# Optimization experiments

Measured on AMD Instinct MI355X. Metric: run time of the kernel, lower is better.

Reference implementation:

```python
import jax, jax.numpy as jnp
import numpy as np

B, S, D, M = 8, 32, 256, 2048
TOPK = 8

def setup_inputs() -> dict:
    key = jax.random.key(0)
    ks = jax.random.split(key, 10)
    def lin(kw, fan_in, fan_out):
        # kaiming normal (linear): std = 1/sqrt(fan_in); stored as [in, out]
        return jax.random.normal(kw, (fan_in, fan_out), jnp.float32) / jnp.sqrt(fan_in)
    return {
        "x": jax.random.normal(ks[0], (B, S, D), jnp.float32),
        "memory": jax.random.normal(ks[1], (M, D), jnp.float32) * 0.02,
        "Wq": lin(ks[2], D, D), "bq": jnp.zeros((D,), jnp.float32),
        "Wk": lin(ks[3], D, D), "bk": jnp.zeros((D,), jnp.float32),
        "Wv": lin(ks[4], D, D), "bv": jnp.zeros((D,), jnp.float32),
        "Wg": lin(ks[5], 2 * D, D), "bg": jnp.zeros((D,), jnp.float32),
    }

def reference(x, memory, Wq, bq, Wk, bk, Wv, bv, Wg, bg):
    batch, seq_len, d = x.shape
    scale = jnp.sqrt(jnp.float32(d))
    mem0 = jnp.broadcast_to(memory[None], (batch,) + memory.shape)  # [B,M,D]
    b_idx = jnp.arange(batch)[:, None]

    def step(mem, xt):  # mem [B,M,D], xt [B,D]
        q = xt @ Wq + bq                      # [B,D]
        k = mem @ Wk + bk                     # [B,M,D]
        v = mem @ Wv + bv                     # [B,M,D]
        logits = jnp.einsum('bd,bmd->bm', q, k) / scale
        attn = jax.nn.softmax(logits, axis=-1)            # [B,M]
        out = jnp.einsum('bm,bmd->bd', attn, v)           # [B,D]
        g = jax.nn.sigmoid(jnp.concatenate([xt, out], axis=-1) @ Wg + bg)  # [B,D]
        _, top_idx = jax.lax.top_k(attn, TOPK)            # [B,TOPK]
        old = jnp.take_along_axis(mem, top_idx[:, :, None], axis=1)        # [B,TOPK,D]
        new = (1.0 - g)[:, None, :] * old + g[:, None, :] * xt[:, None, :]
        mem = mem.at[b_idx, top_idx].set(new)
        return mem, out

    _, outs = jax.lax.scan(step, mem0, jnp.swapaxes(x, 0, 1))  # outs [S,B,D]
    return jnp.swapaxes(outs, 0, 1)  # [B,S,D]
```

## Files before the change

### kernel.cpp

```cpp
#include <hip/hip_runtime.h>
#include <math.h>

constexpr int B_ = 8, S_ = 32, D_ = 256, M_ = 2048;
constexpr int N_ = S_ * B_;
constexpr int TK = 8;
constexpr int NSLOT = 256;
constexpr int TOPC = 256;
constexpr int NCAND = NSLOT + TOPC;
constexpr int KSPLIT = 4;

__global__ __launch_bounds__(256) void k_wvwgT(const float* __restrict__ Wv,
                                               const float* __restrict__ Wg,
                                               const float* __restrict__ bv,
                                               const float* __restrict__ bg,
                                               const float* __restrict__ Wk,
                                               float* __restrict__ WvWgB,
                                               float* __restrict__ bvg,
                                               float* __restrict__ WkT) {
  int blk = blockIdx.x;
  int tid = threadIdx.x;
  if (blk >= 17) {
    __shared__ float tile[32][33];
    int bb = blk - 17;
    int bx = bb & 7, by = bb >> 3;
    int x0 = bx * 32, y0 = by * 32;
    int tx = tid & 31, ty = tid >> 5;
    for (int j = ty; j < 32; j += 8) tile[j][tx] = Wk[(y0 + j) * D_ + x0 + tx];
    __syncthreads();
    for (int j = ty; j < 32; j += 8) WkT[(x0 + j) * D_ + y0 + tx] = tile[tx][j];
    return;
  }
  if (blk == 16) {
    float a = bg[tid];
#pragma unroll 8
    for (int j = 0; j < D_; ++j) a = fmaf(bv[j], Wg[(size_t)(D_ + j) * D_ + tid], a);
    bvg[tid] = a;
    return;
  }
  int i0 = (blk & 3) * 64, d0 = (blk >> 2) * 64;
  __shared__ float At[64 * 64];
  __shared__ float Bt[64 * 64];
  const int r = tid & 63, c = tid >> 6;
  const int lane = tid & 63, wvv = tid >> 6;
  const int tx = lane & 15, ty = lane >> 4;
  const int dg = tx * 4, ig = (wvv * 4 + ty) * 4;
  float acc[4][4];
#pragma unroll
  for (int i = 0; i < 4; ++i)
#pragma unroll
    for (int j = 0; j < 4; ++j) acc[i][j] = 0.f;
  for (int kc = 0; kc < 4; ++kc) {
    __syncthreads();
#pragma unroll
    for (int it = 0; it < 4; ++it) {
      int jq = (c * 4 + it) * 4;
      float4 a = *(const float4*)&Wv[(i0 + r) * D_ + kc * 64 + jq];
      At[(jq + 0) * 64 + r] = a.x; At[(jq + 1) * 64 + r] = a.y;
      At[(jq + 2) * 64 + r] = a.z; At[(jq + 3) * 64 + r] = a.w;
      *(float4*)&Bt[r * 64 + jq] =
          *(const float4*)&Wg[(size_t)(D_ + kc * 64 + r) * D_ + d0 + jq];
    }
    __syncthreads();
#pragma unroll 4
    for (int j = 0; j < 64; ++j) {
      float4 av = *(const float4*)&At[j * 64 + ig];
      float4 bv4 = *(const float4*)&Bt[j * 64 + dg];
      acc[0][0] = fmaf(av.x, bv4.x, acc[0][0]); acc[0][1] = fmaf(av.x, bv4.y, acc[0][1]);
      acc[0][2] = fmaf(av.x, bv4.z, acc[0][2]); acc[0][3] = fmaf(av.x, bv4.w, acc[0][3]);
      acc[1][0] = fmaf(av.y, bv4.x, acc[1][0]); acc[1][1] = fmaf(av.y, bv4.y, acc[1][1]);
      acc[1][2] = fmaf(av.y, bv4.z, acc[1][2]); acc[1][3] = fmaf(av.y, bv4.w, acc[1][3]);
      acc[2][0] = fmaf(av.z, bv4.x, acc[2][0]); acc[2][1] = fmaf(av.z, bv4.y, acc[2][1]);
      acc[2][2] = fmaf(av.z, bv4.z, acc[2][2]); acc[2][3] = fmaf(av.z, bv4.w, acc[2][3]);
      acc[3][0] = fmaf(av.w, bv4.x, acc[3][0]); acc[3][1] = fmaf(av.w, bv4.y, acc[3][1]);
      acc[3][2] = fmaf(av.w, bv4.z, acc[3][2]); acc[3][3] = fmaf(av.w, bv4.w, acc[3][3]);
    }
  }
#pragma unroll
  for (int i = 0; i < 4; ++i)
    *(float4*)&WvWgB[(size_t)(i0 + ig + i) * D_ + d0 + dg] =
        make_float4(acc[i][0], acc[i][1], acc[i][2], acc[i][3]);
}

__global__ __launch_bounds__(256) void k_qproj(
    const float* __restrict__ x, const float* __restrict__ Wq,
    const float* __restrict__ bq, const float* __restrict__ bk,
    const float* __restrict__ WkT, const float* __restrict__ Wg,
    float* __restrict__ qt, float* __restrict__ qbk, float* __restrict__ xgp) {
  int n = blockIdx.x, tid = threadIdx.x;
  int t = n / B_, b = n % B_;
  __shared__ float xr[D_], qsh[D_];
  __shared__ float red[4];
  xr[tid] = x[(b * S_ + t) * D_ + tid];
  __syncthreads();
  float accq = bq[tid], accg = 0.f;
#pragma unroll 8
  for (int i = 0; i < D_; ++i) {
    float xv = xr[i];
    accq = fmaf(xv, Wq[i * D_ + tid], accq);
    accg = fmaf(xv, Wg[i * D_ + tid], accg);
  }
  qsh[tid] = accq;
  xgp[n * D_ + tid] = accg;
  float p = accq * bk[tid];
  for (int off = 32; off > 0; off >>= 1) p += __shfl_down(p, off, 64);
  if ((tid & 63) == 0) red[tid >> 6] = p;
  __syncthreads();
  float acct = 0.f;
#pragma unroll 8
  for (int i = 0; i < D_; ++i) acct = fmaf(qsh[i], WkT[i * D_ + tid], acct);
  qt[n * D_ + tid] = acct;
  if (tid == 0) qbk[n] = red[0] + red[1] + red[2] + red[3];
}

__global__ __launch_bounds__(256) void k_L0(
    const float* __restrict__ qt, const float* __restrict__ mem,
    const float* __restrict__ qbk, float* __restrict__ L0) {
  __shared__ float qtT[64 * 64];
  __shared__ float mT[64 * 64];
  const int tid = threadIdx.x;
  const int m0 = blockIdx.x * 64, n0 = blockIdx.y * 64;
  const int r = tid & 63, c = tid >> 6;
  const int lane = tid & 63, wv = tid >> 6;
  const int tx = lane & 15, ty = lane >> 4;
  const int mg = tx * 4, ng = (wv * 4 + ty) * 4;
  float acc[4][4];
#pragma unroll
  for (int i = 0; i < 4; ++i)
#pragma unroll
    for (int j = 0; j < 4; ++j) acc[i][j] = 0.f;
  for (int kc = 0; kc < 4; ++kc) {
    __syncthreads();
#pragma unroll
    for (int it = 0; it < 4; ++it) {
      int kq = (c * 4 + it) * 4;
      float4 a = *(const float4*)&qt[(n0 + r) * D_ + kc * 64 + kq];
      qtT[(kq + 0) * 64 + r] = a.x; qtT[(kq + 1) * 64 + r] = a.y;
      qtT[(kq + 2) * 64 + r] = a.z; qtT[(kq + 3) * 64 + r] = a.w;
      float4 bm = *(const float4*)&mem[(m0 + r) * D_ + kc * 64 + kq];
      mT[(kq + 0) * 64 + r] = bm.x; mT[(kq + 1) * 64 + r] = bm.y;
      mT[(kq + 2) * 64 + r] = bm.z; mT[(kq + 3) * 64 + r] = bm.w;
    }
    __syncthreads();
#pragma unroll 4
    for (int k = 0; k < 64; ++k) {
      float4 av = *(const float4*)&qtT[k * 64 + ng];
      float4 bv4 = *(const float4*)&mT[k * 64 + mg];
      acc[0][0] = fmaf(av.x, bv4.x, acc[0][0]); acc[0][1] = fmaf(av.x, bv4.y, acc[0][1]);
      acc[0][2] = fmaf(av.x, bv4.z, acc[0][2]); acc[0][3] = fmaf(av.x, bv4.w, acc[0][3]);
      acc[1][0] = fmaf(av.y, bv4.x, acc[1][0]); acc[1][1] = fmaf(av.y, bv4.y, acc[1][1]);
      acc[1][2] = fmaf(av.y, bv4.z, acc[1][2]); acc[1][3] = fmaf(av.y, bv4.w, acc[1][3]);
      acc[2][0] = fmaf(av.z, bv4.x, acc[2][0]); acc[2][1] = fmaf(av.z, bv4.y, acc[2][1]);
      acc[2][2] = fmaf(av.z, bv4.z, acc[2][2]); acc[2][3] = fmaf(av.z, bv4.w, acc[2][3]);
      acc[3][0] = fmaf(av.w, bv4.x, acc[3][0]); acc[3][1] = fmaf(av.w, bv4.y, acc[3][1]);
      acc[3][2] = fmaf(av.w, bv4.z, acc[3][2]); acc[3][3] = fmaf(av.w, bv4.w, acc[3][3]);
    }
  }
#pragma unroll
  for (int i = 0; i < 4; ++i) {
    int n = n0 + ng + i;
    float qbv = qbk[n];
    float4 o;
    o.x = (acc[i][0] + qbv) * 0.0625f; o.y = (acc[i][1] + qbv) * 0.0625f;
    o.z = (acc[i][2] + qbv) * 0.0625f; o.w = (acc[i][3] + qbv) * 0.0625f;
    *(float4*)&L0[n * M_ + m0 + mg] = o;
  }
}

__global__ __launch_bounds__(256) void k_sortstats(const float* __restrict__ L0,
                                                   float* __restrict__ topv,
                                                   int* __restrict__ topi,
                                                   float* __restrict__ M0,
                                                   double* __restrict__ SumE0) {
  int n = blockIdx.x, tid = threadIdx.x;
  __shared__ float v[M_];
  __shared__ short ix[M_];
  __shared__ double redd[4];
  for (int m = tid; m < M_; m += 256) {
    v[m] = L0[(size_t)n * M_ + m];
    ix[m] = (short)m;
  }
  __syncthreads();
  for (int size = 2; size <= M_; size <<= 1) {
    for (int stride = size >> 1; stride > 0; stride >>= 1) {
      for (int i = tid; i < M_ / 2; i += 256) {
        int pos = 2 * i - (i & (stride - 1));
        int j = pos + stride;
        bool desc = ((pos & size) == 0);
        float va = v[pos], vb2 = v[j];
        short ia = ix[pos], ib = ix[j];
        bool aG = (va > vb2) || (va == vb2 && ia < ib);
        if (desc ? !aG : aG) { v[pos] = vb2; v[j] = va; ix[pos] = ib; ix[j] = ia; }
      }
      __syncthreads();
    }
  }
  topv[n * TOPC + tid] = v[tid];
  topi[n * TOPC + tid] = (int)ix[tid];
  float mx = v[0];
  if (tid == 0) M0[n] = mx;
  double s = 0.0;
  for (int m = tid; m < M_; m += 256) s += (double)expf(v[m] - mx);
  for (int off = 32; off > 0; off >>= 1) s += __shfl_down(s, off, 64);
  if ((tid & 63) == 0) redd[tid >> 6] = s;
  __syncthreads();
  if (tid == 0) SumE0[n] = redd[0] + redd[1] + redd[2] + redd[3];
}

__global__ __launch_bounds__(256) void k_ctxpart(
    const float* __restrict__ L0, const float* __restrict__ M0,
    const float* __restrict__ mem, float* __restrict__ ctxp) {
  int ks = blockIdx.x;
  int n0 = blockIdx.y * 32;
  int d0 = blockIdx.z * 64;
  int tid = threadIdx.x;
  __shared__ float Et[64 * 32];
  __shared__ float mTl[64 * 64];
  __shared__ float Msh[32];
  if (tid < 32) Msh[tid] = M0[n0 + tid];
  const int lane = tid & 63, wv = tid >> 6;
  const int tx = lane & 15, ty = lane >> 4;
  const int ng = (wv * 4 + ty) * 2;
  const int dg = tx * 4;
  float acc[2][4] = {{0, 0, 0, 0}, {0, 0, 0, 0}};
  for (int kc = 0; kc < 8; ++kc) {
    int kb = ks * 512 + kc * 64;
    __syncthreads();
#pragma unroll
    for (int j = 0; j < 8; ++j) {
      int ii = tid + 256 * j;
      int nr = ii & 31, kk = ii >> 5;
      Et[kk * 32 + nr] = expf(L0[(n0 + nr) * M_ + kb + kk] - Msh[nr]);
    }
    {
      int r = tid & 63, c = tid >> 6;
#pragma unroll
      for (int j = 0; j < 4; ++j) {
        int c4 = (c * 4 + j) * 4;
        *(float4*)&mTl[r * 64 + c4] = *(const float4*)&mem[(kb + r) * D_ + d0 + c4];
      }
    }
    __syncthreads();
#pragma unroll 4
    for (int kk = 0; kk < 64; ++kk) {
      float4 mv = *(const float4*)&mTl[kk * 64 + dg];
      float e0v = Et[kk * 32 + ng], e1v = Et[kk * 32 + ng + 1];
      acc[0][0] = fmaf(e0v, mv.x, acc[0][0]); acc[0][1] = fmaf(e0v, mv.y, acc[0][1]);
      acc[0][2] = fmaf(e0v, mv.z, acc[0][2]); acc[0][3] = fmaf(e0v, mv.w, acc[0][3]);
      acc[1][0] = fmaf(e1v, mv.x, acc[1][0]); acc[1][1] = fmaf(e1v, mv.y, acc[1][1]);
      acc[1][2] = fmaf(e1v, mv.z, acc[1][2]); acc[1][3] = fmaf(e1v, mv.w, acc[1][3]);
    }
  }
#pragma unroll
  for (int i = 0; i < 2; ++i) {
    int n = n0 + ng + i;
    *(float4*)&ctxp[((size_t)ks * N_ + n) * D_ + d0 + dg] =
        make_float4(acc[i][0], acc[i][1], acc[i][2], acc[i][3]);
  }
}

__global__ __launch_bounds__(1024, 1) void k_scan(
    const float* __restrict__ x, const float* __restrict__ mem0,
    const float* __restrict__ Wv, const float* __restrict__ bv,
    const float* __restrict__ WvWgB, const float* __restrict__ bvg,
    const float* __restrict__ qt, const float* __restrict__ qbk,
    const float* __restrict__ xgp, const float* __restrict__ L0,
    const float* __restrict__ M0, const double* __restrict__ SumE0,
    const float* __restrict__ ctxp, const float* __restrict__ topv,
    const int* __restrict__ topi, float* __restrict__ memcur,
    float* __restrict__ out) {
  const int b = blockIdx.x;
  const int tid = threadIdx.x;
  const int lane = tid & 63;
  const int wvid = tid >> 6;

  __shared__ short tpos[M_];
  __shared__ int Tlist[NSLOT];
  __shared__ float candV[NCAND];
  __shared__ int candI[NCAND];
  __shared__ float dpart[15][D_];
  __shared__ float fpart[16][D_];
  __shared__ float fpart2[16][D_];
  __shared__ float utmp[TK][D_];
  __shared__ float qt_s[2][D_], xt_s[2][D_];
  __shared__ float CTX0_s[D_], xgp_s[D_], g_s[D_], bv_s[D_], bvg_s[D_];
  __shared__ float wvlds[64 * D_];
  __shared__ float Msc[S_], qbks[S_];
  __shared__ double sum0s[S_];
  __shared__ float redw[15];
  __shared__ float inv_esum;
  __shared__ int Tcount;
  __shared__ int selIdx[TK], selSlot[TK], selFresh[TK];

  const float4* mem04 = (const float4*)mem0;
  const float4* mcur4c = (const float4*)memcur;
  float4* mcur4 = (float4*)memcur;
  const float4* Wv4 = (const float4*)Wv;
  const float4* Wg4 = (const float4*)WvWgB;
  const float4* qt4 = (const float4*)qt;
  const float4* x4 = (const float4*)x;
  const float4* ctxp4 = (const float4*)ctxp;
  const float4* xgp4 = (const float4*)xgp;

  float4 wreg[16];
#pragma unroll
  for (int j = 0; j < 16; ++j) wreg[j] = Wv4[(size_t)(wvid * 16 + j) * 64 + lane];

  for (int m = tid; m < M_; m += 1024) tpos[m] = -1;
  for (int i = tid; i < 64 * 64; i += 1024)
    ((float4*)wvlds)[i] = Wg4[192 * 64 + i];
  if (tid < NCAND) {
    candV[tid] = -INFINITY;
    candI[tid] = 0x7FFFFFFF;
  }
  if (tid < S_) {
    Msc[tid] = M0[tid * B_ + b];
    qbks[tid] = qbk[tid * B_ + b];
    sum0s[tid] = SumE0[tid * B_ + b];
  } else if (tid >= 64 && tid < 64 + D_) {
    int d = tid - 64;
    bv_s[d] = bv[d];
    bvg_s[d] = bvg[d];
  } else if (tid >= 512 && tid < 576) {
    int j = tid - 512;
    ((float4*)qt_s[0])[j] = qt4[(size_t)b * 64 + j];
  } else if (tid >= 576 && tid < 640) {
    int j = tid - 576;
    ((float4*)xt_s[0])[j] = x4[(size_t)(b * S_) * 64 + j];
  }
  if (tid == 0) Tcount = 0;
  __syncthreads();

  for (int t = 0; t < S_; ++t) {
    const int n = t * B_ + b;
    const int par = t & 1;
    const int Tc = Tcount;
    const float c0 = Msc[t];
    const float qb = qbks[t];

    if (wvid < 15) {
      const float4 qv = ((const float4*)qt_s[par])[lane];
      float4 acc = make_float4(0.f, 0.f, 0.f, 0.f);
      float dsum = 0.f;
      int s = wvid;
      int m_c = 0;
      float4 mc_c = make_float4(0.f, 0.f, 0.f, 0.f), mo_c = mc_c;
      float l0_c = 0.f;
      if (s < Tc) {
        m_c = Tlist[s];
        mc_c = mcur4c[((size_t)(b * NSLOT + s)) * 64 + lane];
        mo_c = mem04[(size_t)m_c * 64 + lane];
        l0_c = L0[(size_t)n * M_ + m_c];
      }
      while (s < Tc) {
        const int s2 = s + 15;
        int m_n = 0;
        float4 mc_n = make_float4(0.f, 0.f, 0.f, 0.f), mo_n = mc_n;
        float l0_n = 0.f;
        if (s2 < Tc) {
          m_n = Tlist[s2];
          mc_n = mcur4c[((size_t)(b * NSLOT + s2)) * 64 + lane];
          mo_n = mem04[(size_t)m_n * 64 + lane];
          l0_n = L0[(size_t)n * M_ + m_n];
        }
        float p = mc_c.x * qv.x;
        p = fmaf(mc_c.y, qv.y, p);
        p = fmaf(mc_c.z, qv.z, p);
        p = fmaf(mc_c.w, qv.w, p);
#pragma unroll
        for (int off = 1; off < 64; off <<= 1) p += __shfl_xor(p, off, 64);
        const float cur = (p + qb) * 0.0625f;
        const float ce = expf(cur - c0);
        const float e0 = expf(l0_c - c0);
        acc.x = fmaf(ce, mc_c.x, acc.x); acc.x = fmaf(-e0, mo_c.x, acc.x);
        acc.y = fmaf(ce, mc_c.y, acc.y); acc.y = fmaf(-e0, mo_c.y, acc.y);
        acc.z = fmaf(ce, mc_c.z, acc.z); acc.z = fmaf(-e0, mo_c.z, acc.z);
        acc.w = fmaf(ce, mc_c.w, acc.w); acc.w = fmaf(-e0, mo_c.w, acc.w);
        dsum += ce - e0;
        if (lane == 0) {
          candV[s] = cur;
          candI[s] = m_c;
        }
        m_c = m_n; mc_c = mc_n; mo_c = mo_n; l0_c = l0_n;
        s = s2;
      }
      ((float4*)dpart[wvid])[lane] = acc;
      if (lane == 0) redw[wvid] = dsum;
    } else {
#pragma unroll
      for (int jj = 0; jj < 4; ++jj) {
        const int j = lane + jj * 64;
        const int ii = topi[n * TOPC + j];
        const bool fresh = (tpos[ii] < 0);
        candV[NSLOT + j] = fresh ? topv[n * TOPC + j] : -INFINITY;
        candI[NSLOT + j] = fresh ? ii : 0x7FFFFFFF;
      }
      const float4 c0v = ctxp4[(size_t)(0 * N_ + n) * 64 + lane];
      const float4 c1v = ctxp4[(size_t)(1 * N_ + n) * 64 + lane];
      const float4 c2v = ctxp4[(size_t)(2 * N_ + n) * 64 + lane];
      const float4 c3v = ctxp4[(size_t)(3 * N_ + n) * 64 + lane];
      ((float4*)CTX0_s)[lane] = make_float4(c0v.x + c1v.x + c2v.x + c3v.x,
                                            c0v.y + c1v.y + c2v.y + c3v.y,
                                            c0v.z + c1v.z + c2v.z + c3v.z,
                                            c0v.w + c1v.w + c2v.w + c3v.w);
      ((float4*)xgp_s)[lane] = xgp4[(size_t)n * 64 + lane];
      if (t + 1 < S_) {
        ((float4*)qt_s[par ^ 1])[lane] = qt4[(size_t)(n + B_) * 64 + lane];
        ((float4*)xt_s[par ^ 1])[lane] = x4[(size_t)(b * S_ + t + 1) * 64 + lane];
      }
    }
    __syncthreads();

    {
      float mynum = 0.f;
      if (lane < 16) {
        const int k = wvid * 16 + lane;
        float nv = CTX0_s[k];
#pragma unroll
        for (int p = 0; p < 15; ++p) nv += dpart[p][k];
        mynum = nv;
      }
      if (wvid == 15) {
        if (t + 1 < S_) {
          float cv[8];
          int ci[8];
#pragma unroll
          for (int j = 0; j < 8; ++j) {
            cv[j] = candV[lane * 8 + j];
            ci[j] = candI[lane * 8 + j];
          }
          for (int r = 0; r < TK; ++r) {
            float bvv = cv[0];
            int bii = ci[0];
#pragma unroll
            for (int j = 1; j < 8; ++j)
              if (cv[j] > bvv || (cv[j] == bvv && ci[j] < bii)) { bvv = cv[j]; bii = ci[j]; }
#pragma unroll
            for (int off = 1; off < 64; off <<= 1) {
              float ov = __shfl_xor(bvv, off, 64);
              int oi = __shfl_xor(bii, off, 64);
              if (ov > bvv || (ov == bvv && oi < bii)) { bvv = ov; bii = oi; }
            }
            if (lane == 0) selIdx[r] = bii;
#pragma unroll
            for (int j = 0; j < 8; ++j)
              if (ci[j] == bii) { cv[j] = -INFINITY; ci[j] = 0x7FFFFFFF; }
          }
          if (lane == 0) {
            int tc = Tcount;
            for (int k = 0; k < TK; ++k) {
              int m = selIdx[k];
              int s = tpos[m];
              if (s < 0) {
                s = tc++;
                tpos[m] = (short)s;
                Tlist[s] = m;
                selFresh[k] = 1;
              } else
                selFresh[k] = 0;
              selSlot[k] = s;
            }
            Tcount = tc;
          }
        }
        double ds = sum0s[t];
#pragma unroll
        for (int p = 0; p < 15; ++p) ds += (double)redw[p];
        if (lane == 0) inv_esum = (float)(1.0 / ds);
      }
      float4 a1 = make_float4(0.f, 0.f, 0.f, 0.f);
      float4 a2 = make_float4(0.f, 0.f, 0.f, 0.f);
      if (wvid >= 12) {
        const float4* wl = (const float4*)wvlds + (size_t)(wvid - 12) * 16 * 64;
#pragma unroll
        for (int j = 0; j < 16; ++j) {
          const float nv = __shfl(mynum, j, 64);
          a1.x = fmaf(nv, wreg[j].x, a1.x); a1.y = fmaf(nv, wreg[j].y, a1.y);
          a1.z = fmaf(nv, wreg[j].z, a1.z); a1.w = fmaf(nv, wreg[j].w, a1.w);
          const float4 w4 = wl[j * 64 + lane];
          a2.x = fmaf(nv, w4.x, a2.x); a2.y = fmaf(nv, w4.y, a2.y);
          a2.z = fmaf(nv, w4.z, a2.z); a2.w = fmaf(nv, w4.w, a2.w);
        }
      } else {
#pragma unroll
        for (int j = 0; j < 16; ++j) {
          const float nv = __shfl(mynum, j, 64);
          a1.x = fmaf(nv, wreg[j].x, a1.x); a1.y = fmaf(nv, wreg[j].y, a1.y);
          a1.z = fmaf(nv, wreg[j].z, a1.z); a1.w = fmaf(nv, wreg[j].w, a1.w);
          const float4 w4 = Wg4[(size_t)(wvid * 16 + j) * 64 + lane];
          a2.x = fmaf(nv, w4.x, a2.x); a2.y = fmaf(nv, w4.y, a2.y);
          a2.z = fmaf(nv, w4.z, a2.z); a2.w = fmaf(nv, w4.w, a2.w);
        }
      }
      ((float4*)fpart[wvid])[lane] = a1;
      ((float4*)fpart2[wvid])[lane] = a2;
    }
    __syncthreads();

    if (tid < D_) {
      float o = 0.f;
#pragma unroll
      for (int p = 0; p < 16; ++p) o += fpart[p][tid];
      o = o * inv_esum + bv_s[tid];
      out[((size_t)b * S_ + t) * D_ + tid] = o;
    } else if (tid < 2 * D_) {
      const int d = tid - D_;
      float gg = 0.f;
#pragma unroll
      for (int p = 0; p < 16; ++p) gg += fpart2[p][d];
      const float gin = xgp_s[d] + gg * inv_esum + bvg_s[d];
      g_s[d] = 1.0f / (1.0f + expf(-gin));
    } else if (tid >= 512 && t + 1 < S_) {
      const int j = tid - 512, k = j >> 6, l = j & 63;
      const int m = selIdx[k], s = selSlot[k];
      const float4 old4 = selFresh[k] ? mem04[(size_t)m * 64 + l]
                                      : mcur4c[((size_t)(b * NSLOT + s)) * 64 + l];
      ((float4*)utmp[k])[l] = old4;
    }
    __syncthreads();

    if (t + 1 < S_) {
      if (tid < 512) {
        const int k = tid >> 6, l = tid & 63;
        const int s = selSlot[k];
        const float4 old4 = ((const float4*)utmp[k])[l];
        const float4 g4 = ((const float4*)g_s)[l];
        const float4 xv = ((const float4*)xt_s[par])[l];
        float4 nw;
        nw.x = (1.0f - g4.x) * old4.x + g4.x * xv.x;
        nw.y = (1.0f - g4.y) * old4.y + g4.y * xv.y;
        nw.z = (1.0f - g4.z) * old4.z + g4.z * xv.z;
        nw.w = (1.0f - g4.w) * old4.w + g4.w * xv.w;
        mcur4[((size_t)(b * NSLOT + s)) * 64 + l] = nw;
      }
      __syncthreads();
    }
  }
}

extern "C" void kernel_launch(void* const* d_in, const int* in_sizes, int n_in,
                              void* d_out, int out_size, void* d_ws, size_t ws_size,
                              hipStream_t stream) {
  const float* x = (const float*)d_in[0];
  const float* mem0 = (const float*)d_in[1];
  const float* Wq = (const float*)d_in[2];
  const float* bq = (const float*)d_in[3];
  const float* Wk = (const float*)d_in[4];
  const float* bk = (const float*)d_in[5];
  const float* Wv = (const float*)d_in[6];
  const float* bv = (const float*)d_in[7];
  const float* Wg = (const float*)d_in[8];
  const float* bg = (const float*)d_in[9];
  float* out = (float*)d_out;
  float* ws = (float*)d_ws;

  size_t o = 0;
  float* WkT = ws + o;   o += (size_t)D_ * D_;
  float* qt = ws + o;    o += (size_t)N_ * D_;
  float* qbk = ws + o;   o += N_;
  float* xgp = ws + o;   o += (size_t)N_ * D_;
  float* L0 = ws + o;    o += (size_t)N_ * M_;
  float* M0 = ws + o;    o += N_;
  double* SumE0 = (double*)(ws + o); o += 2 * N_;
  float* ctxp = ws + o;  o += (size_t)KSPLIT * N_ * D_;
  float* topv = ws + o;  o += (size_t)N_ * TOPC;
  int* topi = (int*)(ws + o); o += (size_t)N_ * TOPC;
  float* WvWgB = ws + o; o += (size_t)D_ * D_;
  float* bvg = ws + o;   o += D_;
  float* memcur = ws + o; o += (size_t)B_ * NSLOT * D_;

  k_wvwgT<<<dim3(81), dim3(256), 0, stream>>>(Wv, Wg, bv, bg, Wk, WvWgB, bvg, WkT);
  k_qproj<<<dim3(N_), dim3(256), 0, stream>>>(x, Wq, bq, bk, WkT, Wg, qt, qbk, xgp);
  k_L0<<<dim3(M_ / 64, N_ / 64), dim3(256), 0, stream>>>(qt, mem0, qbk, L0);
  k_sortstats<<<dim3(N_), dim3(256), 0, stream>>>(L0, topv, topi, M0, SumE0);
  k_ctxpart<<<dim3(KSPLIT, N_ / 32, D_ / 64), dim3(256), 0, stream>>>(L0, M0, mem0, ctxp);
  k_scan<<<dim3(B_), dim3(1024), 0, stream>>>(x, mem0, Wv, bv, WvWgB, bvg, qt, qbk, xgp,
                                              L0, M0, SumE0, ctxp, topv, topi, memcur, out);
}
```

Baseline: 655.1 us.

## Defer memory slot updates into next step and restructure scan dot-product phase

The top-k memory row update is now deferred and fused into the next step's logit pass: each wave applies the pending gate blend as it loads the row, which removes two block-wide barriers and the utmp staging. The full 64-lane dot-product reduction becomes a 4-lane partial reduce written to LDS and summed per slot by separate threads. The corrections against the original memory rows move to 12 otherwise idle waves, and top-k selection runs in parallel with the accumulation. A new pre-kernel precomputes exp(L0 - max) so the scan does no exp per touched slot; in exchange it writes an extra N*M buffer and adds a barrier phase per step.

Result: slower. 799.1 us (+22.0%).

```diff
diff --git a/kernel.cpp b/kernel.cpp
--- a/kernel.cpp
+++ b/kernel.cpp
@@ -204,6 +204,19 @@
   if ((tid & 63) == 0) redd[tid >> 6] = s;
   __syncthreads();
   if (tid == 0) SumE0[n] = redd[0] + redd[1] + redd[2] + redd[3];
+}
+
+__global__ __launch_bounds__(256) void k_e0(const float* __restrict__ L0,
+                                            const float* __restrict__ M0,
+                                            float* __restrict__ E0all) {
+  int n = blockIdx.x;
+  float c = M0[n];
+  const float4* src = (const float4*)(L0 + (size_t)n * M_);
+  float4* dst = (float4*)(E0all + (size_t)n * M_);
+  for (int j = threadIdx.x; j < M_ / 4; j += 256) {
+    float4 v = src[j];
+    dst[j] = make_float4(expf(v.x - c), expf(v.y - c), expf(v.z - c), expf(v.w - c));
+  }
 }
 
 __global__ __launch_bounds__(256) void k_ctxpart(
@@ -263,7 +276,7 @@
     const float* __restrict__ Wv, const float* __restrict__ bv,
     const float* __restrict__ WvWgB, const float* __restrict__ bvg,
     const float* __restrict__ qt, const float* __restrict__ qbk,
-    const float* __restrict__ xgp, const float* __restrict__ L0,
+    const float* __restrict__ xgp, const float* __restrict__ E0all,
     const float* __restrict__ M0, const double* __restrict__ SumE0,
     const float* __restrict__ ctxp, const float* __restrict__ topv,
     const int* __restrict__ topi, float* __restrict__ memcur,
@@ -275,21 +288,22 @@
 
   __shared__ short tpos[M_];
   __shared__ int Tlist[NSLOT];
+  __shared__ int pendK[NSLOT];
   __shared__ float candV[NCAND];
   __shared__ int candI[NCAND];
-  __shared__ float dpart[15][D_];
+  __shared__ float pLDS[NSLOT * 17];
+  __shared__ float curE[NSLOT], e0sA[NSLOT], diffA[NSLOT];
+  __shared__ float dpart[16][D_];
   __shared__ float fpart[16][D_];
   __shared__ float fpart2[16][D_];
-  __shared__ float utmp[TK][D_];
   __shared__ float qt_s[2][D_], xt_s[2][D_];
   __shared__ float CTX0_s[D_], xgp_s[D_], g_s[D_], bv_s[D_], bvg_s[D_];
   __shared__ float wvlds[64 * D_];
   __shared__ float Msc[S_], qbks[S_];
   __shared__ double sum0s[S_];
-  __shared__ float redw[15];
   __shared__ float inv_esum;
   __shared__ int Tcount;
-  __shared__ int selIdx[TK], selSlot[TK], selFresh[TK];
+  __shared__ int selIdx[TK], selFresh[TK];
 
   const float4* mem04 = (const float4*)mem0;
   const float4* mcur4c = (const float4*)memcur;
@@ -306,6 +320,7 @@
   for (int j = 0; j < 16; ++j) wreg[j] = Wv4[(size_t)(wvid * 16 + j) * 64 + lane];
 
   for (int m = tid; m < M_; m += 1024) tpos[m] = -1;
+  for (int s = tid; s < NSLOT; s += 1024) pendK[s] = -1;
   for (int i = tid; i < 64 * 64; i += 1024)
     ((float4*)wvlds)[i] = Wg4[192 * 64 + i];
   if (tid < NCAND) {
@@ -336,55 +351,57 @@
     const int Tc = Tcount;
     const float c0 = Msc[t];
     const float qb = qbks[t];
+    const float* E0row = E0all + (size_t)n * M_;
 
     if (wvid < 15) {
       const float4 qv = ((const float4*)qt_s[par])[lane];
-      float4 acc = make_float4(0.f, 0.f, 0.f, 0.f);
-      float dsum = 0.f;
+      const float4 g4 = ((const float4*)g_s)[lane];
+      const float4 xpv = ((const float4*)xt_s[par ^ 1])[lane];
       int s = wvid;
-      int m_c = 0;
-      float4 mc_c = make_float4(0.f, 0.f, 0.f, 0.f), mo_c = mc_c;
-      float l0_c = 0.f;
       if (s < Tc) {
-        m_c = Tlist[s];
-        mc_c = mcur4c[((size_t)(b * NSLOT + s)) * 64 + lane];
-        mo_c = mem04[(size_t)m_c * 64 + lane];
-        l0_c = L0[(size_t)n * M_ + m_c];
-      }
-      while (s < Tc) {
-        const int s2 = s + 15;
-        int m_n = 0;
-        float4 mc_n = make_float4(0.f, 0.f, 0.f, 0.f), mo_n = mc_n;
-        float l0_n = 0.f;
-        if (s2 < Tc) {
-          m_n = Tlist[s2];
-          mc_n = mcur4c[((size_t)(b * NSLOT + s2)) * 64 + lane];
-          mo_n = mem04[(size_t)m_n * 64 + lane];
-          l0_n = L0[(size_t)n * M_ + m_n];
+        int m_c = Tlist[s];
+        int pk_c = pendK[s];
+        const float4* base_c = (pk_c >= 0 && selFresh[pk_c])
+                                   ? (mem04 + (size_t)m_c * 64)
+                                   : (mcur4c + ((size_t)(b * NSLOT + s)) * 64);
+        float4 row_c = base_c[lane];
+        while (true) {
+          const int s2 = s + 15;
+          int m_n = 0, pk_n = -1;
+          float4 row_n = make_float4(0.f, 0.f, 0.f, 0.f);
+          if (s2 < Tc) {
+            m_n = Tlist[s2];
+            pk_n = pendK[s2];
+            const float4* base_n = (pk_n >= 0 && selFresh[pk_n])
+                                       ? (mem04 + (size_t)m_n * 64)
+                                       : (mcur4c + ((size_t)(b * NSLOT + s2)) * 64);
+            row_n = base_n[lane];
+          }
+          float4 mc = row_c;
+          if (pk_c >= 0) {
+            mc.x = (1.0f - g4.x) * row_c.x + g4.x * xpv.x;
+            mc.y = (1.0f - g4.y) * row_c.y + g4.y * xpv.y;
+            mc.z = (1.0f - g4.z) * row_c.z + g4.z * xpv.z;
+            mc.w = (1.0f - g4.w) * row_c.w + g4.w * xpv.w;
+            mcur4[((size_t)(b * NSLOT + s)) * 64 + lane] = mc;
+            if (lane == 0) pendK[s] = -1;
+          }
+          float p = mc.x * qv.x;
+          p = fmaf(mc.y, qv.y, p);
+          p = fmaf(mc.z, qv.z, p);
+          p = fmaf(mc.w, qv.w, p);
+          p += __shfl_xor(p, 1, 64);
+          p += __shfl_xor(p, 2, 64);
+          if ((lane & 3) == 0) pLDS[s * 17 + (lane >> 2)] = p;
+          if (lane == 1) e0sA[s] = E0row[m_c];
+          if (lane == 2) candI[s] = m_c;
+          if (s2 >= Tc) break;
+          s = s2;
+          m_c = m_n;
+          pk_c = pk_n;
+          row_c = row_n;
         }
-        float p = mc_c.x * qv.x;
-        p = fmaf(mc_c.y, qv.y, p);
-        p = fmaf(mc_c.z, qv.z, p);
-        p = fmaf(mc_c.w, qv.w, p);
-#pragma unroll
-        for (int off = 1; off < 64; off <<= 1) p += __shfl_xor(p, off, 64);
-        const float cur = (p + qb) * 0.0625f;
-        const float ce = expf(cur - c0);
-        const float e0 = expf(l0_c - c0);
-        acc.x = fmaf(ce, mc_c.x, acc.x); acc.x = fmaf(-e0, mo_c.x, acc.x);
-        acc.y = fmaf(ce, mc_c.y, acc.y); acc.y = fmaf(-e0, mo_c.y, acc.y);
-        acc.z = fmaf(ce, mc_c.z, acc.z); acc.z = fmaf(-e0, mo_c.z, acc.z);
-        acc.w = fmaf(ce, mc_c.w, acc.w); acc.w = fmaf(-e0, mo_c.w, acc.w);
-        dsum += ce - e0;
-        if (lane == 0) {
-          candV[s] = cur;
-          candI[s] = m_c;
-        }
-        m_c = m_n; mc_c = mc_n; mo_c = mo_n; l0_c = l0_n;
-        s = s2;
-      }
-      ((float4*)dpart[wvid])[lane] = acc;
-      if (lane == 0) redw[wvid] = dsum;
+      }
     } else {
 #pragma unroll
       for (int jj = 0; jj < 4; ++jj) {
@@ -410,62 +427,103 @@
     }
     __syncthreads();
 
+    float4 accw = make_float4(0.f, 0.f, 0.f, 0.f);
+    if (tid < NSLOT) {
+      const int s = tid;
+      if (s < Tc) {
+        float dsum = 0.f;
+#pragma unroll
+        for (int j = 0; j < 16; ++j) dsum += pLDS[s * 17 + j];
+        const float cur = (dsum + qb) * 0.0625f;
+        const float ce = expf(cur - c0);
+        const float e0 = e0sA[s];
+        curE[s] = ce;
+        diffA[s] = ce - e0;
+        candV[s] = cur;
+      }
+    } else {
+      for (int s = wvid - 4; s < Tc; s += 12) {
+        const int m = Tlist[s];
+        const float e0 = e0sA[s];
+        const float4 mo = mem04[(size_t)m * 64 + lane];
+        accw.x = fmaf(-e0, mo.x, accw.x);
+        accw.y = fmaf(-e0, mo.y, accw.y);
+        accw.z = fmaf(-e0, mo.z, accw.z);
+        accw.w = fmaf(-e0, mo.w, accw.w);
+      }
+    }
+    __syncthreads();
+
+    if (wvid < 15) {
+      float4 acc = accw;
+      for (int s = wvid; s < Tc; s += 15) {
+        const float ce = curE[s];
+        const float4 mc = mcur4c[((size_t)(b * NSLOT + s)) * 64 + lane];
+        acc.x = fmaf(ce, mc.x, acc.x);
+        acc.y = fmaf(ce, mc.y, acc.y);
+        acc.z = fmaf(ce, mc.z, acc.z);
+        acc.w = fmaf(ce, mc.w, acc.w);
+      }
+      ((float4*)dpart[wvid])[lane] = acc;
+    } else {
+      ((float4*)dpart[15])[lane] = accw;
+      double ds = 0.0;
+      for (int s = lane; s < Tc; s += 64) ds += (double)diffA[s];
+      for (int off = 32; off > 0; off >>= 1) ds += __shfl_down(ds, off, 64);
+      if (lane == 0) inv_esum = (float)(1.0 / (sum0s[t] + ds));
+      if (t + 1 < S_) {
+        float cv[8];
+        int ci[8];
+#pragma unroll
+        for (int j = 0; j < 8; ++j) {
+          cv[j] = candV[lane * 8 + j];
+          ci[j] = candI[lane * 8 + j];
+        }
+        for (int r = 0; r < TK; ++r) {
+          float bvv = cv[0];
+          int bii = ci[0];
+#pragma unroll
+          for (int j = 1; j < 8; ++j)
+            if (cv[j] > bvv || (cv[j] == bvv && ci[j] < bii)) { bvv = cv[j]; bii = ci[j]; }
+#pragma unroll
+          for (int off = 1; off < 64; off <<= 1) {
+            float ov = __shfl_xor(bvv, off, 64);
+            int oi = __shfl_xor(bii, off, 64);
+            if (ov > bvv || (ov == bvv && oi < bii)) { bvv = ov; bii = oi; }
+          }
+          if (lane == 0) selIdx[r] = bii;
+#pragma unroll
+          for (int j = 0; j < 8; ++j)
+            if (ci[j] == bii) { cv[j] = -INFINITY; ci[j] = 0x7FFFFFFF; }
+        }
+        if (lane == 0) {
+          int tc = Tcount;
+          for (int k = 0; k < TK; ++k) {
+            const int m = selIdx[k];
+            int s = tpos[m];
+            if (s < 0) {
+              s = tc++;
+              tpos[m] = (short)s;
+              Tlist[s] = m;
+              selFresh[k] = 1;
+            } else
+              selFresh[k] = 0;
+            pendK[s] = k;
+          }
+          Tcount = tc;
+        }
+      }
+    }
+    __syncthreads();
+
     {
       float mynum = 0.f;
       if (lane < 16) {
         const int k = wvid * 16 + lane;
         float nv = CTX0_s[k];
 #pragma unroll
-        for (int p = 0; p < 15; ++p) nv += dpart[p][k];
+        for (int p = 0; p < 16; ++p) nv += dpart[p][k];
         mynum = nv;
-      }
-      if (wvid == 15) {
-        if (t + 1 < S_) {
-          float cv[8];
-          int ci[8];
-#pragma unroll
-          for (int j = 0; j < 8; ++j) {
-            cv[j] = candV[lane * 8 + j];
-            ci[j] = candI[lane * 8 + j];
-          }
-          for (int r = 0; r < TK; ++r) {
-            float bvv = cv[0];
-            int bii = ci[0];
-#pragma unroll
-            for (int j = 1; j < 8; ++j)
-              if (cv[j] > bvv || (cv[j] == bvv && ci[j] < bii)) { bvv = cv[j]; bii = ci[j]; }
-#pragma unroll
-            for (int off = 1; off < 64; off <<= 1) {
-              float ov = __shfl_xor(bvv, off, 64);
-              int oi = __shfl_xor(bii, off, 64);
-              if (ov > bvv || (ov == bvv && oi < bii)) { bvv = ov; bii = oi; }
-            }
-            if (lane == 0) selIdx[r] = bii;
-#pragma unroll
-            for (int j = 0; j < 8; ++j)
-              if (ci[j] == bii) { cv[j] = -INFINITY; ci[j] = 0x7FFFFFFF; }
-          }
-          if (lane == 0) {
-            int tc = Tcount;
-            for (int k = 0; k < TK; ++k) {
-              int m = selIdx[k];
-              int s = tpos[m];
-              if (s < 0) {
-                s = tc++;
-                tpos[m] = (short)s;
-                Tlist[s] = m;
-                selFresh[k] = 1;
-              } else
-                selFresh[k] = 0;
-              selSlot[k] = s;
-            }
-            Tcount = tc;
-          }
-        }
-        double ds = sum0s[t];
-#pragma unroll
-        for (int p = 0; p < 15; ++p) ds += (double)redw[p];
-        if (lane == 0) inv_esum = (float)(1.0 / ds);
       }
       float4 a1 = make_float4(0.f, 0.f, 0.f, 0.f);
       float4 a2 = make_float4(0.f, 0.f, 0.f, 0.f);
@@ -509,31 +567,8 @@
       for (int p = 0; p < 16; ++p) gg += fpart2[p][d];
       const float gin = xgp_s[d] + gg * inv_esum + bvg_s[d];
       g_s[d] = 1.0f / (1.0f + expf(-gin));
-    } else if (tid >= 512 && t + 1 < S_) {
-      const int j = tid - 512, k = j >> 6, l = j & 63;
-      const int m = selIdx[k], s = selSlot[k];
-      const float4 old4 = selFresh[k] ? mem04[(size_t)m * 64 + l]
-                                      : mcur4c[((size_t)(b * NSLOT + s)) * 64 + l];
-      ((float4*)utmp[k])[l] = old4;
-    }
-    __syncthreads();
-
-    if (t + 1 < S_) {
-      if (tid < 512) {
-        const int k = tid >> 6, l = tid & 63;
-        const int s = selSlot[k];
-        const float4 old4 = ((const float4*)utmp[k])[l];
-        const float4 g4 = ((const float4*)g_s)[l];
-        const float4 xv = ((const float4*)xt_s[par])[l];
-        float4 nw;
-        nw.x = (1.0f - g4.x) * old4.x + g4.x * xv.x;
-        nw.y = (1.0f - g4.y) * old4.y + g4.y * xv.y;
-        nw.z = (1.0f - g4.z) * old4.z + g4.z * xv.z;
-        nw.w = (1.0f - g4.w) * old4.w + g4.w * xv.w;
-        mcur4[((size_t)(b * NSLOT + s)) * 64 + l] = nw;
-      }
-      __syncthreads();
-    }
+    }
+    __syncthreads();
   }
 }
 
@@ -554,25 +589,27 @@
   float* ws = (float*)d_ws;
 
   size_t o = 0;
-  float* WkT = ws + o;   o += (size_t)D_ * D_;
-  float* qt = ws + o;    o += (size_t)N_ * D_;
-  float* qbk = ws + o;   o += N_;
-  float* xgp = ws + o;   o += (size_t)N_ * D_;
-  float* L0 = ws + o;    o += (size_t)N_ * M_;
-  float* M0 = ws + o;    o += N_;
+  float* WkT = ws + o;    o += (size_t)D_ * D_;
+  float* qt = ws + o;     o += (size_t)N_ * D_;
+  float* qbk = ws + o;    o += N_;
+  float* xgp = ws + o;    o += (size_t)N_ * D_;
+  float* L0 = ws + o;     o += (size_t)N_ * M_;
+  float* M0 = ws + o;     o += N_;
   double* SumE0 = (double*)(ws + o); o += 2 * N_;
-  float* ctxp = ws + o;  o += (size_t)KSPLIT * N_ * D_;
-  float* topv = ws + o;  o += (size_t)N_ * TOPC;
+  float* ctxp = ws + o;   o += (size_t)KSPLIT * N_ * D_;
+  float* topv = ws + o;   o += (size_t)N_ * TOPC;
   int* topi = (int*)(ws + o); o += (size_t)N_ * TOPC;
-  float* WvWgB = ws + o; o += (size_t)D_ * D_;
-  float* bvg = ws + o;   o += D_;
+  float* WvWgB = ws + o;  o += (size_t)D_ * D_;
+  float* bvg = ws + o;    o += D_;
+  float* E0all = ws + o;  o += (size_t)N_ * M_;
   float* memcur = ws + o; o += (size_t)B_ * NSLOT * D_;
 
   k_wvwgT<<<dim3(81), dim3(256), 0, stream>>>(Wv, Wg, bv, bg, Wk, WvWgB, bvg, WkT);
   k_qproj<<<dim3(N_), dim3(256), 0, stream>>>(x, Wq, bq, bk, WkT, Wg, qt, qbk, xgp);
   k_L0<<<dim3(M_ / 64, N_ / 64), dim3(256), 0, stream>>>(qt, mem0, qbk, L0);
   k_sortstats<<<dim3(N_), dim3(256), 0, stream>>>(L0, topv, topi, M0, SumE0);
+  k_e0<<<dim3(N_), dim3(256), 0, stream>>>(L0, M0, E0all);
   k_ctxpart<<<dim3(KSPLIT, N_ / 32, D_ / 64), dim3(256), 0, stream>>>(L0, M0, mem0, ctxp);
   k_scan<<<dim3(B_), dim3(1024), 0, stream>>>(x, mem0, Wv, bv, WvWgB, bvg, qt, qbk, xgp,
-                                              L0, M0, SumE0, ctxp, topv, topi, memcur, out);
-}
+                                              E0all, M0, SumE0, ctxp, topv, topi, memcur, out);
+}
```
